# Kernel optimization log

Measured on AMD Instinct MI355X. Metric: run time of the kernel, lower is better.

The kernel has to match this reference:

```python
import math
import jax, jax.numpy as jnp
import numpy as np

EPS = 1e-5  # BatchNorm2d default eps


def setup_inputs() -> dict:
    key = jax.random.key(0)
    ks = jax.random.split(key, 12)
    C, I = 256, 128  # in_channels, inter_channels (= C // reduction)
    n, h, w = 4, 64, 64
    s = 0.02
    return {
        "x": jax.random.normal(ks[0], (n, C, h, w), jnp.float32),
        "g_w": jax.random.normal(ks[1], (I, C), jnp.float32) * s,
        "g_b": jax.random.normal(ks[2], (I,), jnp.float32) * s,
        "theta_w": jax.random.normal(ks[3], (I, C), jnp.float32) * s,
        "theta_b": jax.random.normal(ks[4], (I,), jnp.float32) * s,
        "phi_w": jax.random.normal(ks[5], (I, C), jnp.float32) * s,
        "phi_b": jax.random.normal(ks[6], (I,), jnp.float32) * s,
        "out_w": jax.random.normal(ks[7], (C, I), jnp.float32) * s,
        "bn_gamma": jax.random.uniform(ks[8], (C,), jnp.float32, 0.5, 1.5),
        "bn_beta": jax.random.normal(ks[9], (C,), jnp.float32) * s,
        "bn_mean": jax.random.normal(ks[10], (C,), jnp.float32) * s,
        "bn_var": jax.random.uniform(ks[11], (C,), jnp.float32, 0.5, 1.5),
    }


def reference(x, g_w, g_b, theta_w, theta_b, phi_w, phi_b, out_w,
              bn_gamma, bn_beta, bn_mean, bn_var):
    n, c, h, w = x.shape
    xf = x.reshape(n, c, h * w)  # (n, C, N)

    def proj(Wm, b):  # 1x1 conv == per-position linear: (n, I, N)
        return jnp.einsum('ic,ncp->nip', Wm, xf) + b[None, :, None]

    g_x = proj(g_w, g_b)          # (n, I, N)
    theta_x = proj(theta_w, theta_b)  # (n, I, N)
    phi_x = proj(phi_w, phi_b)        # (n, I, N)

    # dot_product mode: softmax FIRST, then divide by sqrt(C) (faithful to source)
    scores = jnp.einsum('nip,niq->npq', theta_x, phi_x)  # (n, N, N)
    attn = jax.nn.softmax(scores, axis=-1) / math.sqrt(c)

    y = jnp.einsum('npq,niq->nip', attn, g_x)  # (n, I, N)
    y = y.reshape(n, -1, h, w)                 # (n, I, h, w)

    # conv_out: 1x1 conv (no bias) + BatchNorm2d (eval-mode running stats)
    y = jnp.einsum('oi,nihw->nohw', out_w, y)  # (n, C, h, w)
    inv = bn_gamma / jnp.sqrt(bn_var + EPS)
    y = y * inv[None, :, None, None] + (bn_beta - bn_mean * inv)[None, :, None, None]
    return y + x
```

## Files before the change

### kernel.cpp

```cpp
#include <hip/hip_runtime.h>

typedef short short8 __attribute__((ext_vector_type(8)));
typedef short short4v __attribute__((ext_vector_type(4)));
typedef float f32x4 __attribute__((ext_vector_type(4)));
typedef float f32x16 __attribute__((ext_vector_type(16)));
typedef unsigned int uint4v __attribute__((ext_vector_type(4)));
typedef unsigned int uint2v __attribute__((ext_vector_type(2)));

#define NB 4
#define CD 256
#define ID 128
#define NP 4096

static __device__ __forceinline__ short f2bf(float f){
  unsigned u = __float_as_uint(f);
  u += 0x7FFF + ((u >> 16) & 1);
  return (short)(u >> 16);
}
static __device__ __forceinline__ float bf2f(short s){
  unsigned u = ((unsigned)(unsigned short)s) << 16;
  return __uint_as_float(u);
}
static __device__ __forceinline__ unsigned cvtpk(float lo, float hi){
  unsigned r;
  asm("v_cvt_pk_bf16_f32 %0, %1, %2" : "=v"(r) : "v"(lo), "v"(hi));
  return r;
}
static __device__ __forceinline__ float fexp2(float x){
  float r;
  asm("v_exp_f32 %0, %1" : "=v"(r) : "v"(x));
  return r;
}
static __device__ __forceinline__ unsigned pack4_fp8(float a, float b, float c, float d){
  unsigned lo, hi;
  asm("v_cvt_pk_fp8_f32 %0, %1, %2" : "=v"(lo) : "v"(a), "v"(b));
  asm("v_cvt_pk_fp8_f32 %0, %1, %2" : "=v"(hi) : "v"(c), "v"(d));
  return (lo & 0xffffu) | (hi << 16);
}
static __device__ __forceinline__ unsigned char f2fp8(float v){
  unsigned u;
  asm("v_cvt_pk_fp8_f32 %0, %1, %1" : "=v"(u) : "v"(v));
  return (unsigned char)u;
}

static __device__ __forceinline__ void gload16(const void* g, void* l){
  __builtin_amdgcn_global_load_lds(
      (const __attribute__((address_space(1))) unsigned int*)g,
      (__attribute__((address_space(3))) unsigned int*)l, 16, 0, 0);
}

__global__ __launch_bounds__(256) void k_cvtw(const float* __restrict__ g_w,
    const float* __restrict__ th_w, const float* __restrict__ ph_w,
    const float* __restrict__ out_w, short* __restrict__ wb){
  int idx = (blockIdx.x * 256 + threadIdx.x) * 4;
  const float* s;
  int sel = idx >> 15;
  if(sel == 0) s = g_w; else if(sel == 1) s = th_w; else if(sel == 2) s = ph_w; else s = out_w;
  int off = idx & 32767;
  float4 v = *reinterpret_cast<const float4*>(s + off);
  short4v o = { f2bf(v.x), f2bf(v.y), f2bf(v.z), f2bf(v.w) };
  *reinterpret_cast<short4v*>(wb + idx) = o;
}

__global__ __launch_bounds__(256) void k_transpose(const float* __restrict__ x,
                                                   short* __restrict__ xt){
  __shared__ float T[64][68];
  int n = blockIdx.z, c0 = blockIdx.y * 64, p0 = blockIdx.x * 64;
  int t = threadIdx.x;
  const float* xp = x + ((size_t)(n * CD + c0)) * NP + p0;
#pragma unroll
  for(int it = 0; it < 4; ++it){
    int c = (t >> 4) + it * 16;
    int p = (t & 15) * 4;
    float4 v = *reinterpret_cast<const float4*>(xp + (size_t)c * NP + p);
    T[c][p+0] = v.x; T[c][p+1] = v.y; T[c][p+2] = v.z; T[c][p+3] = v.w;
  }
  __syncthreads();
  short* op = xt + ((size_t)(n * NP + p0)) * CD + c0;
  int p = t >> 2, cc = (t & 3) * 16;
  short8 a, b;
#pragma unroll
  for(int j = 0; j < 8; ++j){ a[j] = f2bf(T[cc + j][p]); b[j] = f2bf(T[cc + 8 + j][p]); }
  *reinterpret_cast<short8*>(op + (size_t)p * CD + cc) = a;
  *reinterpret_cast<short8*>(op + (size_t)p * CD + cc + 8) = b;
}

__global__ __launch_bounds__(512) void k_proj(const short* __restrict__ xt,
    const short* __restrict__ wb, const float* __restrict__ g_b,
    const float* __restrict__ th_b, const float* __restrict__ ph_b,
    unsigned char* __restrict__ q8, unsigned char* __restrict__ k8,
    unsigned char* __restrict__ v8){
  __shared__ __align__(16) char XT[32768];
  int b = blockIdx.x;
  int n = b >> 6, pt = b & 63;
  int pb0 = pt * 64;
  int t = threadIdx.x, w = t >> 6, l = t & 63;
  int lr = l & 15, lg = l >> 4;
  int i0 = w * 16;

  const char* xg = (const char*)(xt + ((size_t)(n * NP + pb0)) * CD);
#pragma unroll
  for(int i_ = 0; i_ < 4; ++i_){
    int dd = t * 16 + i_ * 8192;
    int row = dd >> 9;
    int sz = (dd & ~511) | ((dd & 511) ^ ((row & 15) << 4));
    gload16(xg + sz, XT + dd);
  }

  const short* gww = wb;
  const short* thw = wb + 32768;
  const short* phw = wb + 65536;
  short8 Wt[8], Wp[8], Wg[8];
#pragma unroll
  for(int kk = 0; kk < 8; ++kk){
    size_t wo = (size_t)(i0 + lr) * CD + kk * 32 + lg * 8;
    Wt[kk] = *reinterpret_cast<const short8*>(thw + wo);
    Wp[kk] = *reinterpret_cast<const short8*>(phw + wo);
    Wg[kk] = *reinterpret_cast<const short8*>(gww + wo);
  }
  float bt = th_b[i0 + lr];
  float bp = ph_b[i0 + lr];
  int ik = i0 + lr;
  int ip = (ik & 7) | (((ik >> 4) & 1) << 3) | (((ik >> 3) & 1) << 4) | ((ik >> 5) << 5);
  float gb[4];
#pragma unroll
  for(int r = 0; r < 4; ++r) gb[r] = g_b[i0 + lg * 4 + r];

  __syncthreads();

  size_t vbase = ((size_t)n * 64 + pt) * 8192;
#pragma unroll
  for(int psub = 0; psub < 4; ++psub){
    int prow = psub * 16 + lr;
    short8 X[8];
#pragma unroll
    for(int kk = 0; kk < 8; ++kk)
      X[kk] = *reinterpret_cast<const short8*>(
          XT + prow * 512 + ((kk * 64 + lg * 16) ^ ((prow & 15) << 4)));
    f32x4 aT = {0.f,0.f,0.f,0.f}, aP = {0.f,0.f,0.f,0.f}, aG = {0.f,0.f,0.f,0.f};
#pragma unroll
    for(int kk = 0; kk < 8; ++kk){
      aT = __builtin_amdgcn_mfma_f32_16x16x32_bf16(X[kk], Wt[kk], aT, 0, 0, 0);
      aP = __builtin_amdgcn_mfma_f32_16x16x32_bf16(X[kk], Wp[kk], aP, 0, 0, 0);
      aG = __builtin_amdgcn_mfma_f32_16x16x32_bf16(Wg[kk], X[kk], aG, 0, 0, 0);
    }
#pragma unroll
    for(int r = 0; r < 4; ++r){
      size_t row = (size_t)(n * NP + pb0 + psub * 16 + lg * 4 + r);
      q8[row * ID + i0 + lr] = f2fp8((aT[r] + bt) * 1.44269504f);
      k8[row * ID + ip]      = f2fp8(aP[r] + bp);
    }
#pragma unroll
    for(int r = 0; r < 4; ++r){
      int ii = i0 + lg * 4 + r;
      v8[vbase + (psub >> 1) * 4096 + ((lr >> 3) & 1) * 2048 + ii * 16
               + (psub & 1) * 8 + (lr & 7)] = f2fp8(aG[r] + gb[r]);
    }
  }
}

__global__ __launch_bounds__(256, 2) void k_attn(const unsigned char* __restrict__ q8,
    const unsigned char* __restrict__ k8, const unsigned char* __restrict__ v8,
    short* __restrict__ po, float* __restrict__ psums){
  __shared__ __align__(16) char smem[65536];
  int b = blockIdx.x;
  int xcd = b & 7;
  int n = xcd >> 1;
  int kq = ((xcd & 1) << 1) | ((b >> 3) & 1);
  int qtl = b >> 4;
  int t = threadIdx.x, w = t >> 6, l = t & 63;
  int q31 = l & 31, hi = l >> 5;
  int pbase = qtl * 128 + w * 32;

  const char* kpanel = (const char*)k8 + ((size_t)(n * NP + kq * 1024)) * ID;
  const char* vpanel = (const char*)v8 + ((size_t)n * 64 + kq * 16) * 8192;
  const char* qbase  = (const char*)q8 + ((size_t)(n * NP + pbase)) * ID;

  uint2v Qf[8];
#pragma unroll
  for(int cst = 0; cst < 8; ++cst)
    Qf[cst] = *reinterpret_cast<const uint2v*>(qbase + q31 * 128 + cst * 16 + hi * 8);

  f32x16 Of[4];
#pragma unroll
  for(int db = 0; db < 4; ++db)
#pragma unroll
    for(int r = 0; r < 16; ++r) Of[db][r] = 0.f;
  float ps = 0.f;

#define STAGE(cb, kt_) do { \
    const char* kg_ = kpanel + (size_t)(kt_) * 8192; \
    const char* vg_ = vpanel + (size_t)(kt_) * 8192; \
    char* kld_ = smem + (cb) * 8192; \
    char* vld_ = smem + 16384 + (cb) * 8192; \
    _Pragma("unroll") \
    for(int i_ = 0; i_ < 2; ++i_){ \
      int dd = t * 16 + i_ * 4096; \
      int ks = (((dd >> 4) & 63) << 7) | ((dd >> 11) << 5) | (((dd >> 10) & 1) << 4); \
      gload16(kg_ + ks, kld_ + dd); \
      gload16(vg_ + dd, vld_ + dd); \
    } \
  } while(0)

  STAGE(0, 0);
  __syncthreads();

#pragma unroll 2
  for(int kt = 0; kt < 16; ++kt){
    const int pb = kt & 1;
    if(kt + 1 < 16) STAGE(pb ^ 1, kt + 1);
    const char* Kc = smem + pb * 8192;
    const char* Vc = smem + 16384 + pb * 8192;
#pragma unroll
    for(int kb = 0; kb < 2; ++kb){
      f32x16 S;
#pragma unroll
      for(int r = 0; r < 16; ++r) S[r] = 0.f;
      int krow = kb * 32 + q31;
      __builtin_amdgcn_s_setprio(1);
#pragma unroll
      for(int cp = 0; cp < 4; ++cp){
        uint4v Kp = *reinterpret_cast<const uint4v*>(
            Kc + cp * 2048 + hi * 1024 + krow * 16);
        uint2v Ka = { Kp[0], Kp[1] };
        uint2v Kb2 = { Kp[2], Kp[3] };
        S = __builtin_amdgcn_mfma_f32_32x32x16_fp8_fp8(
            __builtin_bit_cast(long, Ka), __builtin_bit_cast(long, Qf[2*cp]), S, 0, 0, 0);
        S = __builtin_amdgcn_mfma_f32_32x32x16_fp8_fp8(
            __builtin_bit_cast(long, Kb2), __builtin_bit_cast(long, Qf[2*cp+1]), S, 0, 0, 0);
      }
      __builtin_amdgcn_s_setprio(0);
      float e[16];
#pragma unroll
      for(int r = 0; r < 16; ++r) e[r] = fexp2(S[r] - 4.0f);
#pragma unroll
      for(int r = 0; r < 16; ++r) ps += e[r];
      unsigned u0 = pack4_fp8(e[0],  e[1],  e[2],  e[3]);
      unsigned u1 = pack4_fp8(e[4],  e[5],  e[6],  e[7]);
      unsigned u2 = pack4_fp8(e[8],  e[9],  e[10], e[11]);
      unsigned u3 = pack4_fp8(e[12], e[13], e[14], e[15]);
      asm("v_permlane32_swap_b32 %0, %1" : "+v"(u0), "+v"(u1));
      asm("v_permlane32_swap_b32 %0, %1" : "+v"(u2), "+v"(u3));
      long P0 = __builtin_bit_cast(long, uint2v{u0, u1});
      long P1 = __builtin_bit_cast(long, uint2v{u2, u3});
      __builtin_amdgcn_s_setprio(1);
#pragma unroll
      for(int db = 0; db < 4; ++db){
        int d = db * 32 + q31;
        uint4v Vp = *reinterpret_cast<const uint4v*>(
            Vc + kb * 4096 + hi * 2048 + d * 16);
        uint2v Va = { Vp[0], Vp[1] };
        uint2v Vb = { Vp[2], Vp[3] };
        Of[db] = __builtin_amdgcn_mfma_f32_32x32x16_fp8_fp8(
            P0, __builtin_bit_cast(long, Va), Of[db], 0, 0, 0);
        Of[db] = __builtin_amdgcn_mfma_f32_32x32x16_fp8_fp8(
            P1, __builtin_bit_cast(long, Vb), Of[db], 0, 0, 0);
      }
      __builtin_amdgcn_s_setprio(0);
    }
    __syncthreads();
  }
#undef STAGE

  float pst = ps + __shfl_xor(ps, 32);
  if(hi == 0)
    psums[(size_t)kq * 16384 + n * NP + pbase + q31] = pst;

  float* ow = (float*)(smem + w * 16384);
#pragma unroll
  for(int reg = 0; reg < 16; ++reg){
    int q = (reg & 3) + 8 * (reg >> 2) + 4 * hi;
#pragma unroll
    for(int db = 0; db < 4; ++db)
      ow[q * 128 + db * 32 + q31] = Of[db][reg];
  }
  asm volatile("s_waitcnt lgkmcnt(0)" ::: "memory");
  __builtin_amdgcn_sched_barrier(0);
  short* pr = po + ((size_t)kq * 16384 + n * NP + pbase) * ID;
#pragma unroll
  for(int it = 0; it < 8; ++it){
    int o = it * 1024 + l * 16;
    int q = o >> 8, d0 = (o & 255) >> 1;
    f32x4 va = *reinterpret_cast<const f32x4*>(ow + q * 128 + d0);
    f32x4 vb = *reinterpret_cast<const f32x4*>(ow + q * 128 + d0 + 4);
    uint4v pk4 = { cvtpk(va[0], va[1]), cvtpk(va[2], va[3]),
                   cvtpk(vb[0], vb[1]), cvtpk(vb[2], vb[3]) };
    *reinterpret_cast<short8*>(pr + (size_t)q * ID + d0) = __builtin_bit_cast(short8, pk4);
  }
}

__global__ __launch_bounds__(512) void k_outproj(const short* __restrict__ po,
    const float* __restrict__ psums, const short* __restrict__ ow_b,
    const float* __restrict__ bng, const float* __restrict__ bnb,
    const float* __restrict__ bnm, const float* __restrict__ bnv,
    const float* __restrict__ x, float* __restrict__ out){
  __shared__ __align__(16) short XW[64 * 128];
  int b = blockIdx.x;
  int n = b >> 6, pt = b & 63;
  int pg0 = pt * 64;
  int t = threadIdx.x, w = t >> 6, l = t & 63;
  int lr = l & 15, lg = l >> 4;

  {
    int p = t >> 3, i0 = (t & 7) * 16;
    size_t qg = (size_t)n * NP + pg0 + p;
    float den = psums[qg] + psums[16384 + qg] + psums[32768 + qg] + psums[49152 + qg];
    float inv = 1.f / (16.f * den);
    const short* pp = po + qg * ID + i0;
    int key = (p & 15) << 4;
#pragma unroll
    for(int h = 0; h < 2; ++h){
      short8 b0 = *reinterpret_cast<const short8*>(pp + h * 8);
      short8 b1 = *reinterpret_cast<const short8*>(pp + (size_t)16384 * ID + h * 8);
      short8 b2 = *reinterpret_cast<const short8*>(pp + (size_t)32768 * ID + h * 8);
      short8 b3 = *reinterpret_cast<const short8*>(pp + (size_t)49152 * ID + h * 8);
      float f[8];
#pragma unroll
      for(int j = 0; j < 8; ++j)
        f[j] = (bf2f(b0[j]) + bf2f(b1[j]) + bf2f(b2[j]) + bf2f(b3[j])) * inv;
      uint4v pkv = { cvtpk(f[0], f[1]), cvtpk(f[2], f[3]),
                     cvtpk(f[4], f[5]), cvtpk(f[6], f[7]) };
      *reinterpret_cast<short8*>((char*)XW + p * 256 + ((i0 * 2 + h * 16) ^ key)) =
          __builtin_bit_cast(short8, pkv);
    }
  }
  __syncthreads();

  int c0 = w * 32;
  f32x4 acc[2][4];
#pragma unroll
  for(int mf = 0; mf < 2; ++mf)
#pragma unroll
    for(int nf = 0; nf < 4; ++nf) acc[mf][nf] = {0.f,0.f,0.f,0.f};
#pragma unroll
  for(int kk = 0; kk < 4; ++kk){
    short8 Af[2];
#pragma unroll
    for(int mf = 0; mf < 2; ++mf)
      Af[mf] = *reinterpret_cast<const short8*>(ow_b + (size_t)(c0 + mf * 16 + lr) * ID + kk * 32 + lg * 8);
#pragma unroll
    for(int nf = 0; nf < 4; ++nf){
      int prow = nf * 16 + lr;
      short8 Bf = *reinterpret_cast<const short8*>(
          (char*)XW + prow * 256 + ((kk * 64 + lg * 16) ^ ((prow & 15) << 4)));
#pragma unroll
      for(int mf = 0; mf < 2; ++mf)
        acc[mf][nf] = __builtin_amdgcn_mfma_f32_16x16x32_bf16(Af[mf], Bf, acc[mf][nf], 0, 0, 0);
    }
  }

#pragma unroll
  for(int mf = 0; mf < 2; ++mf){
    int cb = c0 + mf * 16 + lg * 4;
    float inv[4], sh[4];
#pragma unroll
    for(int r = 0; r < 4; ++r){
      float iv = bng[cb + r] * rsqrtf(bnv[cb + r] + 1e-5f);
      inv[r] = iv;
      sh[r] = bnb[cb + r] - bnm[cb + r] * iv;
    }
#pragma unroll
    for(int nf = 0; nf < 4; ++nf){
      int p = pg0 + nf * 16 + lr;
#pragma unroll
      for(int r = 0; r < 4; ++r){
        size_t idx = ((size_t)(n * CD + cb + r)) * NP + p;
        out[idx] = acc[mf][nf][r] * inv[r] + sh[r] + x[idx];
      }
    }
  }
}

extern "C" void kernel_launch(void* const* d_in, const int* in_sizes, int n_in,
                              void* d_out, int out_size, void* d_ws, size_t ws_size,
                              hipStream_t stream){
  const float* x    = (const float*)d_in[0];
  const float* g_w  = (const float*)d_in[1];
  const float* g_b  = (const float*)d_in[2];
  const float* th_w = (const float*)d_in[3];
  const float* th_b = (const float*)d_in[4];
  const float* ph_w = (const float*)d_in[5];
  const float* ph_b = (const float*)d_in[6];
  const float* out_w= (const float*)d_in[7];
  const float* bng  = (const float*)d_in[8];
  const float* bnb  = (const float*)d_in[9];
  const float* bnm  = (const float*)d_in[10];
  const float* bnv  = (const float*)d_in[11];
  float* out = (float*)d_out;
  char* ws = (char*)d_ws;

  short* xt          = (short*)(ws);
  unsigned char* q8  = (unsigned char*)(ws + (size_t)(8u  << 20));
  unsigned char* k8  = (unsigned char*)(ws + (size_t)(12u << 20));
  unsigned char* v8  = (unsigned char*)(ws + (size_t)(16u << 20));
  short* wb          = (short*)(ws + (size_t)(24u << 20));
  short* po          = (short*)(ws + (size_t)(25u << 20));
  float* psum        = (float*)(ws + (size_t)(41u << 20));

  k_cvtw<<<128, 256, 0, stream>>>(g_w, th_w, ph_w, out_w, wb);
  k_transpose<<<dim3(64, 4, 4), 256, 0, stream>>>(x, xt);
  k_proj<<<256, 512, 0, stream>>>(xt, wb, g_b, th_b, ph_b, q8, k8, v8);
  k_attn<<<512, 256, 0, stream>>>(q8, k8, v8, po, psum);
  k_outproj<<<256, 512, 0, stream>>>(po, psum, wb + 98304, bng, bnb, bnm, bnv, x, out);
}
```

Measured before the change: 66.49 us.

## Fuse input transpose into projection kernel and split score MFMA accumulators

Removes the separate transpose kernel: the projection kernel now loads a 256x64 fp32 tile of x straight into LDS, converts and transposes it to bf16 in a swizzled layout, then runs the existing MFMA projections. This drops a launch and the round trip of the bf16 transposed copy through global memory, in exchange for 96KB of LDS per block (lower occupancy) and an extra barrier. Separately, the attention score MFMA chain is split into two independent accumulators that are summed before exp, which shortens the dependency chain between MFMAs at the cost of more registers.

```diff
diff --git a/kernel.cpp b/kernel.cpp
--- a/kernel.cpp
+++ b/kernel.cpp
@@ -62,35 +62,13 @@
   *reinterpret_cast<short4v*>(wb + idx) = o;
 }
 
-__global__ __launch_bounds__(256) void k_transpose(const float* __restrict__ x,
-                                                   short* __restrict__ xt){
-  __shared__ float T[64][68];
-  int n = blockIdx.z, c0 = blockIdx.y * 64, p0 = blockIdx.x * 64;
-  int t = threadIdx.x;
-  const float* xp = x + ((size_t)(n * CD + c0)) * NP + p0;
-#pragma unroll
-  for(int it = 0; it < 4; ++it){
-    int c = (t >> 4) + it * 16;
-    int p = (t & 15) * 4;
-    float4 v = *reinterpret_cast<const float4*>(xp + (size_t)c * NP + p);
-    T[c][p+0] = v.x; T[c][p+1] = v.y; T[c][p+2] = v.z; T[c][p+3] = v.w;
-  }
-  __syncthreads();
-  short* op = xt + ((size_t)(n * NP + p0)) * CD + c0;
-  int p = t >> 2, cc = (t & 3) * 16;
-  short8 a, b;
-#pragma unroll
-  for(int j = 0; j < 8; ++j){ a[j] = f2bf(T[cc + j][p]); b[j] = f2bf(T[cc + 8 + j][p]); }
-  *reinterpret_cast<short8*>(op + (size_t)p * CD + cc) = a;
-  *reinterpret_cast<short8*>(op + (size_t)p * CD + cc + 8) = b;
-}
-
-__global__ __launch_bounds__(512) void k_proj(const short* __restrict__ xt,
+__global__ __launch_bounds__(512) void k_proj(const float* __restrict__ x,
     const short* __restrict__ wb, const float* __restrict__ g_b,
     const float* __restrict__ th_b, const float* __restrict__ ph_b,
     unsigned char* __restrict__ q8, unsigned char* __restrict__ k8,
     unsigned char* __restrict__ v8){
-  __shared__ __align__(16) char XT[32768];
+  __shared__ __align__(16) char smem[98304];
+  char* XT = smem + 65536;
   int b = blockIdx.x;
   int n = b >> 6, pt = b & 63;
   int pb0 = pt * 64;
@@ -98,13 +76,11 @@
   int lr = l & 15, lg = l >> 4;
   int i0 = w * 16;
 
-  const char* xg = (const char*)(xt + ((size_t)(n * NP + pb0)) * CD);
-#pragma unroll
-  for(int i_ = 0; i_ < 4; ++i_){
+  const char* xg = (const char*)(x + ((size_t)n * CD) * NP + pb0);
+#pragma unroll
+  for(int i_ = 0; i_ < 8; ++i_){
     int dd = t * 16 + i_ * 8192;
-    int row = dd >> 9;
-    int sz = (dd & ~511) | ((dd & 511) ^ ((row & 15) << 4));
-    gload16(xg + sz, XT + dd);
+    gload16(xg + (size_t)(dd >> 8) * 16384 + (dd & 255), smem + dd);
   }
 
   const short* gww = wb;
@@ -126,6 +102,26 @@
 #pragma unroll
   for(int r = 0; r < 4; ++r) gb[r] = g_b[i0 + lg * 4 + r];
 
+  __syncthreads();
+
+  {
+    int p = l;
+    const float* src = (const float*)smem;
+    int key = (p & 15) << 4;
+#pragma unroll
+    for(int jj = 0; jj < 4; ++jj){
+      unsigned pk4v[4];
+#pragma unroll
+      for(int q = 0; q < 4; ++q){
+        int cp2 = w * 16 + jj * 4 + q;
+        float f0 = src[(2 * cp2) * 64 + p];
+        float f1 = src[(2 * cp2 + 1) * 64 + p];
+        pk4v[q] = cvtpk(f0, f1);
+      }
+      uint4v v4 = { pk4v[0], pk4v[1], pk4v[2], pk4v[3] };
+      *reinterpret_cast<uint4v*>(XT + p * 512 + ((w * 64 + jj * 16) ^ key)) = v4;
+    }
+  }
   __syncthreads();
 
   size_t vbase = ((size_t)n * 64 + pt) * 8192;
@@ -213,9 +209,9 @@
     const char* Vc = smem + 16384 + pb * 8192;
 #pragma unroll
     for(int kb = 0; kb < 2; ++kb){
-      f32x16 S;
-#pragma unroll
-      for(int r = 0; r < 16; ++r) S[r] = 0.f;
+      f32x16 Sa, Sb;
+#pragma unroll
+      for(int r = 0; r < 16; ++r){ Sa[r] = 0.f; Sb[r] = 0.f; }
       int krow = kb * 32 + q31;
       __builtin_amdgcn_s_setprio(1);
 #pragma unroll
@@ -224,15 +220,15 @@
             Kc + cp * 2048 + hi * 1024 + krow * 16);
         uint2v Ka = { Kp[0], Kp[1] };
         uint2v Kb2 = { Kp[2], Kp[3] };
-        S = __builtin_amdgcn_mfma_f32_32x32x16_fp8_fp8(
-            __builtin_bit_cast(long, Ka), __builtin_bit_cast(long, Qf[2*cp]), S, 0, 0, 0);
-        S = __builtin_amdgcn_mfma_f32_32x32x16_fp8_fp8(
-            __builtin_bit_cast(long, Kb2), __builtin_bit_cast(long, Qf[2*cp+1]), S, 0, 0, 0);
+        Sa = __builtin_amdgcn_mfma_f32_32x32x16_fp8_fp8(
+            __builtin_bit_cast(long, Ka), __builtin_bit_cast(long, Qf[2*cp]), Sa, 0, 0, 0);
+        Sb = __builtin_amdgcn_mfma_f32_32x32x16_fp8_fp8(
+            __builtin_bit_cast(long, Kb2), __builtin_bit_cast(long, Qf[2*cp+1]), Sb, 0, 0, 0);
       }
       __builtin_amdgcn_s_setprio(0);
       float e[16];
 #pragma unroll
-      for(int r = 0; r < 16; ++r) e[r] = fexp2(S[r] - 4.0f);
+      for(int r = 0; r < 16; ++r) e[r] = fexp2(Sa[r] + Sb[r] - 4.0f);
 #pragma unroll
       for(int r = 0; r < 16; ++r) ps += e[r];
       unsigned u0 = pack4_fp8(e[0],  e[1],  e[2],  e[3]);
@@ -389,7 +385,6 @@
   float* out = (float*)d_out;
   char* ws = (char*)d_ws;
 
-  short* xt          = (short*)(ws);
   unsigned char* q8  = (unsigned char*)(ws + (size_t)(8u  << 20));
   unsigned char* k8  = (unsigned char*)(ws + (size_t)(12u << 20));
   unsigned char* v8  = (unsigned char*)(ws + (size_t)(16u << 20));
@@ -398,8 +393,7 @@
   float* psum        = (float*)(ws + (size_t)(41u << 20));
 
   k_cvtw<<<128, 256, 0, stream>>>(g_w, th_w, ph_w, out_w, wb);
-  k_transpose<<<dim3(64, 4, 4), 256, 0, stream>>>(x, xt);
-  k_proj<<<256, 512, 0, stream>>>(xt, wb, g_b, th_b, ph_b, q8, k8, v8);
+  k_proj<<<256, 512, 0, stream>>>(x, wb, g_b, th_b, ph_b, q8, k8, v8);
   k_attn<<<512, 256, 0, stream>>>(q8, k8, v8, po, psum);
   k_outproj<<<256, 512, 0, stream>>>(po, psum, wb + 98304, bng, bnb, bnm, bnv, x, out);
 }
```

Result: faster. 64.53 us (-3.0%).
